# Optimization experiments

Measured on AMD Instinct MI355X. Metric: run time of the kernel, lower is better.

The kernel has to match this reference:

```python
import jax, jax.numpy as jnp
import numpy as np

EPS = 1e-8  # torch F.cosine_similarity default eps
B, T, D = 128, 32, 256
H = 512            # LSTM hidden
S, M = 2048, 64    # memory slots, mem dim
R, W = 4, 1        # read / write heads
OUT = 256


def setup_inputs() -> dict:
    key = jax.random.key(0)
    ks = jax.random.split(key, 12)
    sc = 0.02
    return {
        "x": jax.random.normal(ks[0], (B, T, D), jnp.float32),
        "h0": jnp.zeros((B, H), jnp.float32),
        "c0": jnp.zeros((B, H), jnp.float32),
        "mem0": jax.random.normal(ks[1], (B, S, M), jnp.float32),
        # LSTMCell params (torch gate order i,f,g,o)
        "W_ih": jax.random.normal(ks[2], (4 * H, D), jnp.float32) * sc,
        "W_hh": jax.random.normal(ks[3], (4 * H, H), jnp.float32) * sc,
        "b_ih": jnp.zeros((4 * H,), jnp.float32),
        "b_hh": jnp.zeros((4 * H,), jnp.float32),
        # linear_output: H -> OUT
        "W_out": jax.random.normal(ks[4], (OUT, H), jnp.float32) * 0.001,
        "b_out": jnp.zeros((OUT,), jnp.float32),
        # output_fn: (R*M) -> OUT
        "W_rd": jax.random.normal(ks[5], (OUT, R * M), jnp.float32) * 0.001,
        "b_rd": jnp.zeros((OUT,), jnp.float32),
        # ctrl2head: H -> R*M + R + W*M + W + W*M + W*M
        "W_head": jax.random.normal(ks[6], (R * M + R + 3 * W * M + W, H), jnp.float32) * 0.001,
        "b_head": jnp.zeros((R * M + R + 3 * W * M + W,), jnp.float32),
        "K": 8,
    }


def asp(t, K):
    # top-K sparse masking over last dim (slots); equals torch topk+scatter
    v, idx = jax.lax.top_k(t, K)                       # [B, h, K]
    b = jnp.arange(t.shape[0])[:, None, None]
    h = jnp.arange(t.shape[1])[None, :, None]
    return jnp.zeros_like(t).at[b, h, idx].set(v)


def content_addressing(mem, k, beta):
    # mem [B,S,M], k [B,h,M], beta [B,h,1] -> softmax(beta * cosine_sim) over slots
    dots = jnp.einsum("bhm,bsm->bhs", k, mem)
    kn = jnp.maximum(jnp.linalg.norm(k, axis=-1), EPS)[:, :, None]      # [B,h,1]
    mn = jnp.maximum(jnp.linalg.norm(mem, axis=-1), EPS)[:, None, :]    # [B,1,S]
    cossim = dots / (kn * mn)
    return jax.nn.softmax(beta * cossim, axis=-1)


def dnc_forward(x, h0, c0, mem0, W_ih, W_hh, b_ih, b_hh,
                W_out, b_out, W_rd, b_rd, W_head, b_head, K):
    def step(carry, x_t):
        h, c, mem = carry
        # LSTM cell
        gates = x_t @ W_ih.T + h @ W_hh.T + (b_ih + b_hh)
        i, f, g, o = jnp.split(gates, 4, axis=-1)
        c = jax.nn.sigmoid(f) * c + jax.nn.sigmoid(i) * jnp.tanh(g)
        h = jax.nn.sigmoid(o) * jnp.tanh(c)
        vt = h @ W_out.T + b_out
        # addressing params
        ctrl = h @ W_head.T + b_head
        s = 0
        kr = jnp.tanh(ctrl[:, s:s + R * M]).reshape(-1, R, M); s += R * M
        betar = jax.nn.softplus(ctrl[:, s:s + R]).reshape(-1, R, 1); s += R
        kw = jnp.tanh(ctrl[:, s:s + W * M]).reshape(-1, W, M); s += W * M
        betaw = jax.nn.softplus(ctrl[:, s:s + W]).reshape(-1, W, 1); s += W
        erase = jax.nn.sigmoid(ctrl[:, s:s + W * M]).reshape(-1, W, M); s += W * M
        add = jnp.tanh(ctrl[:, s:s + W * M]).reshape(-1, W, M)
        # write: sparse content addressing, rank-1 erase/add per write head
        ww = asp(content_addressing(mem, kw, betaw), K)     # [B,W,S]
        e = jnp.einsum("bws,bwm->bwsm", ww, erase)
        a = jnp.einsum("bws,bwm->bwsm", ww, add)
        for widx in range(W):
            mem = mem * (1.0 - e[:, widx]) + a[:, widx]
        # read
        wr = asp(content_addressing(mem, kr, betar), K)     # [B,R,S]
        reads = jnp.einsum("brs,bsm->brm", wr, mem)         # [B,R,M]
        out = vt + reads.reshape(reads.shape[0], -1) @ W_rd.T + b_rd
        return (h, c, mem), out

    (_, _, _), outs = jax.lax.scan(step, (h0, c0, mem0), jnp.swapaxes(x, 0, 1))
    return jnp.swapaxes(outs, 0, 1)  # [B, T, OUT]


def reference(x, h0, c0, mem0, W_ih, W_hh, b_ih, b_hh,
              W_out, b_out, W_rd, b_rd, W_head, b_head, K):
    return dnc_forward(x, h0, c0, mem0, W_ih, W_hh, b_ih, b_hh,
                       W_out, b_out, W_rd, b_rd, W_head, b_head, K)
```

## Files before the change

### kernel.cpp

```cpp
#include <hip/hip_runtime.h>
#include <math.h>

#define DEV __device__ __forceinline__

static constexpr int B_ = 128, T_ = 32, H_ = 512;
static constexpr int S_ = 2048, M_ = 64, OUT_ = 256;
static constexpr float EPSF = 1e-8f;

DEV float sigmoidf_(float x){ return 1.0f/(1.0f+expf(-x)); }
DEV float softplusf_(float x){ return fmaxf(x,0.0f) + log1pf(expf(-fabsf(x))); }

DEV unsigned long long packCand(float v, unsigned idx){
  unsigned u = __float_as_uint(v);
  unsigned m = (u & 0x80000000u) ? ~u : (u | 0x80000000u);
  return ((unsigned long long)m << 32) | (unsigned)(~idx);
}
DEV float unpackVal(unsigned long long e){
  unsigned m = (unsigned)(e >> 32);
  unsigned u = (m & 0x80000000u) ? (m & 0x7FFFFFFFu) : ~m;
  return __uint_as_float(u);
}
DEV unsigned unpackIdx(unsigned long long e){ return ~(unsigned)e; }

DEV void cswp(unsigned long long &a, unsigned long long &b){
  if(a < b){ unsigned long long t=a; a=b; b=t; }
}
DEV void sort8(unsigned long long* L){
  cswp(L[0],L[1]); cswp(L[2],L[3]); cswp(L[4],L[5]); cswp(L[6],L[7]);
  cswp(L[0],L[2]); cswp(L[1],L[3]); cswp(L[4],L[6]); cswp(L[5],L[7]);
  cswp(L[1],L[2]); cswp(L[5],L[6]);
  cswp(L[0],L[4]); cswp(L[1],L[5]); cswp(L[2],L[6]); cswp(L[3],L[7]);
  cswp(L[2],L[4]); cswp(L[3],L[5]);
  cswp(L[1],L[2]); cswp(L[3],L[4]); cswp(L[5],L[6]);
}
DEV void bmerge16(unsigned long long* C){
  #pragma unroll
  for(int i=0;i<8;i++) cswp(C[i],C[i+8]);
  #pragma unroll
  for(int g=0;g<2;g++){ int o=g*8;
    cswp(C[o+0],C[o+4]); cswp(C[o+1],C[o+5]); cswp(C[o+2],C[o+6]); cswp(C[o+3],C[o+7]); }
  #pragma unroll
  for(int g=0;g<4;g++){ int o=g*4; cswp(C[o+0],C[o+2]); cswp(C[o+1],C[o+3]); }
  #pragma unroll
  for(int g=0;g<8;g++){ int o=g*2; cswp(C[o],C[o+1]); }
}
DEV void butterfly8(unsigned long long* L, int maxMask){
  for(int mask=1; mask<=maxMask; mask<<=1){
    unsigned long long O[8], C[8];
    #pragma unroll
    for(int i=0;i<8;i++) O[i] = __shfl_xor(L[i], mask, 64);
    #pragma unroll
    for(int i=0;i<8;i++){ unsigned long long a=L[i], b=O[7-i]; C[i] = (a>b)?a:b; }
    cswp(C[0],C[4]); cswp(C[1],C[5]); cswp(C[2],C[6]); cswp(C[3],C[7]);
    cswp(C[0],C[2]); cswp(C[1],C[3]); cswp(C[4],C[6]); cswp(C[5],C[7]);
    cswp(C[0],C[1]); cswp(C[2],C[3]); cswp(C[4],C[5]); cswp(C[6],C[7]);
    #pragma unroll
    for(int i=0;i<8;i++) L[i]=C[i];
  }
}
DEV void butterfly16(unsigned long long* L){
  for(int mask=1; mask<64; mask<<=1){
    unsigned long long O[16], C[16];
    #pragma unroll
    for(int i=0;i<16;i++) O[i] = __shfl_xor(L[i], mask, 64);
    #pragma unroll
    for(int i=0;i<16;i++){ unsigned long long a=L[i], b=O[15-i]; C[i] = (a>b)?a:b; }
    bmerge16(C);
    #pragma unroll
    for(int i=0;i<16;i++) L[i]=C[i];
  }
}

DEV float ctrlv(const float* __restrict__ cp, int b, int jj, const float* __restrict__ bh){
  size_t o = (size_t)b*512 + jj;
  return cp[o] + cp[65536+o] + cp[131072+o] + cp[196608+o] + bh[jj];
}

__global__ __launch_bounds__(256)
void k_gemm64(const float* __restrict__ A, int lda,
              const float* __restrict__ Bm, int ldb,
              float* __restrict__ C, int ldc,
              int kCount,
              const float* __restrict__ bias0, const float* __restrict__ bias1)
{
  const int BM=64, BN=64, BK=16, LDT=68;
  __shared__ float As[BK*LDT];
  __shared__ float Bs[BK*LDT];
  const int m0 = blockIdx.x*BM, n0 = blockIdx.y*BN;
  const int tid = threadIdx.x;
  const int tx = tid & 15, ty = tid >> 4;
  const int kStart = blockIdx.z * kCount;
  float acc[4][4] = {};
  const int row = tid >> 2, kk = (tid & 3) * 4;
  for(int k0 = kStart; k0 < kStart + kCount; k0 += BK){
    float4 av = *(const float4*)(A  + (size_t)(m0+row)*lda + k0 + kk);
    float4 bv = *(const float4*)(Bm + (size_t)(n0+row)*ldb + k0 + kk);
    As[(kk+0)*LDT+row]=av.x; As[(kk+1)*LDT+row]=av.y; As[(kk+2)*LDT+row]=av.z; As[(kk+3)*LDT+row]=av.w;
    Bs[(kk+0)*LDT+row]=bv.x; Bs[(kk+1)*LDT+row]=bv.y; Bs[(kk+2)*LDT+row]=bv.z; Bs[(kk+3)*LDT+row]=bv.w;
    __syncthreads();
    #pragma unroll
    for(int k=0;k<BK;k++){
      float4 a = *(const float4*)&As[k*LDT + 4*ty];
      float4 b = *(const float4*)&Bs[k*LDT + 4*tx];
      acc[0][0]+=a.x*b.x; acc[0][1]+=a.x*b.y; acc[0][2]+=a.x*b.z; acc[0][3]+=a.x*b.w;
      acc[1][0]+=a.y*b.x; acc[1][1]+=a.y*b.y; acc[1][2]+=a.y*b.z; acc[1][3]+=a.y*b.w;
      acc[2][0]+=a.z*b.x; acc[2][1]+=a.z*b.y; acc[2][2]+=a.z*b.z; acc[2][3]+=a.z*b.w;
      acc[3][0]+=a.w*b.x; acc[3][1]+=a.w*b.y; acc[3][2]+=a.w*b.z; acc[3][3]+=a.w*b.w;
    }
    __syncthreads();
  }
  float* Cz = C + (size_t)blockIdx.z * (size_t)gridDim.x * BM * (size_t)ldc;
  #pragma unroll
  for(int i=0;i<4;i++){
    int m = m0 + 4*ty + i;
    int n = n0 + 4*tx;
    float4 o; o.x=acc[i][0]; o.y=acc[i][1]; o.z=acc[i][2]; o.w=acc[i][3];
    if(bias0){
      o.x += bias0[n]+bias1[n];     o.y += bias0[n+1]+bias1[n+1];
      o.z += bias0[n+2]+bias1[n+2]; o.w += bias0[n+3]+bias1[n+3];
    }
    *(float4*)(Cz + (size_t)m*ldc + n) = o;
  }
}

__global__ __launch_bounds__(256)
void k_L1(const float* __restrict__ hprev, const float* __restrict__ Whh,
          float* __restrict__ gparts, int tG,
          const float* __restrict__ hv,
          const float* __restrict__ Wout, const float* __restrict__ Whead,
          float* __restrict__ ctrlW, float* __restrict__ vtpW, int tV,
          float* __restrict__ memC, const float* __restrict__ ctrlH,
          const float* __restrict__ bhead,
          const unsigned long long* __restrict__ candW,
          const unsigned long long* __restrict__ candR,
          const float* __restrict__ statsB,
          float* __restrict__ readsAll, int tH)
{
  __shared__ __align__(16) float smem[2304];
  const int blk = blockIdx.x, tid = threadIdx.x;

  if(blk < 256){
    if(tG < 0) return;
    float* As = smem;
    float* Bs = smem + 1088;
    const int z = blk >> 6, rem = blk & 63;
    const int m0 = (rem & 1)*64, n0 = (rem >> 1)*64;
    const int tx = tid & 15, ty = tid >> 4;
    float acc[4][4] = {};
    const int row = tid >> 2, kq = (tid & 3)*4;
    const int kStart = z*128;
    for(int k0 = kStart; k0 < kStart + 128; k0 += 16){
      float4 av = *(const float4*)(hprev + (size_t)(m0+row)*512 + k0 + kq);
      float4 bv = *(const float4*)(Whh   + (size_t)(n0+row)*512 + k0 + kq);
      As[(kq+0)*68+row]=av.x; As[(kq+1)*68+row]=av.y; As[(kq+2)*68+row]=av.z; As[(kq+3)*68+row]=av.w;
      Bs[(kq+0)*68+row]=bv.x; Bs[(kq+1)*68+row]=bv.y; Bs[(kq+2)*68+row]=bv.z; Bs[(kq+3)*68+row]=bv.w;
      __syncthreads();
      #pragma unroll
      for(int k=0;k<16;k++){
        float4 a = *(const float4*)&As[k*68 + 4*ty];
        float4 b = *(const float4*)&Bs[k*68 + 4*tx];
        acc[0][0]+=a.x*b.x; acc[0][1]+=a.x*b.y; acc[0][2]+=a.x*b.z; acc[0][3]+=a.x*b.w;
        acc[1][0]+=a.y*b.x; acc[1][1]+=a.y*b.y; acc[1][2]+=a.y*b.z; acc[1][3]+=a.y*b.w;
        acc[2][0]+=a.z*b.x; acc[2][1]+=a.z*b.y; acc[2][2]+=a.z*b.z; acc[2][3]+=a.z*b.w;
        acc[3][0]+=a.w*b.x; acc[3][1]+=a.w*b.y; acc[3][2]+=a.w*b.z; acc[3][3]+=a.w*b.w;
      }
      __syncthreads();
    }
    float* Cz = gparts + (size_t)z*262144;
    #pragma unroll
    for(int i=0;i<4;i++){
      float4 o; o.x=acc[i][0]; o.y=acc[i][1]; o.z=acc[i][2]; o.w=acc[i][3];
      *(float4*)(Cz + (size_t)(m0+4*ty+i)*2048 + n0 + 4*tx) = o;
    }
    return;
  }

  if(blk < 320){
    if(tV < 0) return;
    float* As = smem;
    float* Bs = smem + 1088;
    const int g = blk - 256;
    const int z = g >> 4, rem = g & 15;
    const int m0 = (rem & 1)*64;
    const int jj0 = (rem >> 1)*64;
    const int tx = tid & 15, ty = tid >> 4;
    float acc[4][4] = {};
    const int row = tid >> 2, kq = (tid & 3)*4;
    const int kStart = z*128;
    const int jr = jj0 + row;
    const float* Bsrc = (jr < 453) ? (Whead + (size_t)jr*512) : nullptr;
    for(int k0 = kStart; k0 < kStart + 128; k0 += 16){
      float4 av = *(const float4*)(hv + (size_t)(m0+row)*512 + k0 + kq);
      float4 bv = make_float4(0.f,0.f,0.f,0.f);
      if(Bsrc) bv = *(const float4*)(Bsrc + k0 + kq);
      As[(kq+0)*68+row]=av.x; As[(kq+1)*68+row]=av.y; As[(kq+2)*68+row]=av.z; As[(kq+3)*68+row]=av.w;
      Bs[(kq+0)*68+row]=bv.x; Bs[(kq+1)*68+row]=bv.y; Bs[(kq+2)*68+row]=bv.z; Bs[(kq+3)*68+row]=bv.w;
      __syncthreads();
      #pragma unroll
      for(int k=0;k<16;k++){
        float4 a = *(const float4*)&As[k*68 + 4*ty];
        float4 b = *(const float4*)&Bs[k*68 + 4*tx];
        acc[0][0]+=a.x*b.x; acc[0][1]+=a.x*b.y; acc[0][2]+=a.x*b.z; acc[0][3]+=a.x*b.w;
        acc[1][0]+=a.y*b.x; acc[1][1]+=a.y*b.y; acc[1][2]+=a.y*b.z; acc[1][3]+=a.y*b.w;
        acc[2][0]+=a.z*b.x; acc[2][1]+=a.z*b.y; acc[2][2]+=a.z*b.z; acc[2][3]+=a.z*b.w;
        acc[3][0]+=a.w*b.x; acc[3][1]+=a.w*b.y; acc[3][2]+=a.w*b.z; acc[3][3]+=a.w*b.w;
      }
      __syncthreads();
    }
    float* Cz = ctrlW + (size_t)z*65536;
    #pragma unroll
    for(int i=0;i<4;i++){
      float4 o; o.x=acc[i][0]; o.y=acc[i][1]; o.z=acc[i][2]; o.w=acc[i][3];
      *(float4*)(Cz + (size_t)(m0+4*ty+i)*512 + jj0 + 4*tx) = o;
    }
    return;
  }

  if(blk < 448){
    if(tH < 0) return;
    float* kr     = smem;
    float* nv     = smem + 256;
    float* oldrow = smem + 768;
    float* er     = smem + 1280;
    float* ad     = smem + 1344;
    float* coefR  = smem + 1408;
    int*   widx   = (int*)(smem + 1412);
    float* wval   = smem + 1420;

    const int b = blk - 320;
    const int lane = tid & 63, wave = tid >> 6;
    const size_t memb = (size_t)b*(size_t)S_*M_;

    kr[tid] = tanhf(ctrlv(ctrlH, b, tid, bhead));
    if(tid < 64){
      er[tid] = sigmoidf_(ctrlv(ctrlH, b, 325+tid, bhead));
      ad[tid] = tanhf(ctrlv(ctrlH, b, 389+tid, bhead));
    }
    __syncthreads();

    if(wave == 0){
      float smx[4], ssm[4];
      #pragma unroll
      for(int c2=0;c2<4;c2++){
        const float* st = statsB + (((size_t)b*4 + c2)*5 + 4)*2;
        smx[c2] = st[0]; ssm[c2] = st[1];
      }
      float mxw = fmaxf(fmaxf(smx[0],smx[1]), fmaxf(smx[2],smx[3]));
      float Zw = ssm[0]*expf(smx[0]-mxw) + ssm[1]*expf(smx[1]-mxw)
               + ssm[2]*expf(smx[2]-mxw) + ssm[3]*expf(smx[3]-mxw);
      unsigned long long L[8];
      L[0] = (lane < 32) ? candW[((size_t)b*4 + (lane>>3))*8 + (lane&7)] : 0ULL;
      #pragma unroll
      for(int j=1;j<8;j++) L[j] = 0ULL;
      butterfly8(L, 16);
      if(lane == 0){
        float invZ = 1.0f / Zw;
        #pragma unroll
        for(int p=0;p<8;p++){
          widx[p] = (int)unpackIdx(L[p]);
          wval[p] = expf(unpackVal(L[p]) - mxw) * invZ;
        }
      }
    } else if(wave == 1 && lane < 4){
      float s = 0.f;
      #pragma unroll
      for(int m=0;m<64;m++){ float x = kr[lane*64+m]; s += x*x; }
      coefR[lane] = softplusf_(ctrlv(ctrlH, b, 256+lane, bhead)) / fmaxf(sqrtf(s), EPSF);
    }
    __syncthreads();

    {
      int j = tid >> 6, m = tid & 63;
      #pragma unroll
      for(int p=0;p<2;p++){
        int idx = tid + p*256;
        int jj = idx >> 6, mm = idx & 63;
        int s = widx[jj];
        float w = wval[jj];
        size_t ptr = memb + (size_t)s*M_ + mm;
        float old = memC[ptr];
        oldrow[jj*64+mm] = old;
        float x = old * (1.0f - w*er[mm]) + w*ad[mm];
        memC[ptr] = x;
        nv[jj*64+mm] = x;
      }
      (void)j; (void)m;
    }
    __syncthreads();

    {
      const int r = wave;
      const int sW = lane & 7, g = lane >> 3;
      const float4* nv4 = (const float4*)nv;
      const float4* ov4 = (const float4*)oldrow;
      const float4* kr4 = (const float4*)kr;
      float4 na = nv4[sW*16 + g*2], nb2 = nv4[sW*16 + g*2 + 1];
      float4 oa = ov4[sW*16 + g*2], ob = ov4[sW*16 + g*2 + 1];
      float4 ka = kr4[r*16  + g*2], kb = kr4[r*16  + g*2 + 1];
      float dot = na.x*ka.x + na.y*ka.y + na.z*ka.z + na.w*ka.w
                + nb2.x*kb.x + nb2.y*kb.y + nb2.z*kb.z + nb2.w*kb.w;
      float n2  = na.x*na.x + na.y*na.y + na.z*na.z + na.w*na.w
                + nb2.x*nb2.x + nb2.y*nb2.y + nb2.z*nb2.z + nb2.w*nb2.w;
      float odot= oa.x*ka.x + oa.y*ka.y + oa.z*ka.z + oa.w*ka.w
                + ob.x*kb.x + ob.y*kb.y + ob.z*kb.z + ob.w*kb.w;
      float on2 = oa.x*oa.x + oa.y*oa.y + oa.z*oa.z + oa.w*oa.w
                + ob.x*ob.x + ob.y*ob.y + ob.z*ob.z + ob.w*ob.w;
      #pragma unroll
      for(int mask=8; mask<64; mask<<=1){
        dot  += __shfl_xor(dot,  mask, 64);
        n2   += __shfl_xor(n2,   mask, 64);
        odot += __shfl_xor(odot, mask, 64);
        on2  += __shfl_xor(on2,  mask, 64);
      }
      float fixv = coefR[r] * dot  / fmaxf(sqrtf(n2),  EPSF);
      float oldv = coefR[r] * odot / fmaxf(sqrtf(on2), EPSF);
      int myw = widx[sW];

      float scx[4], scs[4];
      #pragma unroll
      for(int c2=0;c2<4;c2++){
        const float* st = statsB + (((size_t)b*4 + c2)*5 + r)*2;
        scx[c2] = st[0]; scs[c2] = st[1];
      }
      float mxp = fmaxf(fmaxf(scx[0],scx[1]), fmaxf(scx[2],scx[3]));

      unsigned long long L[8];
      {
        int c2 = lane >> 4, rank = lane & 15;
        unsigned long long eA = candR[(((size_t)b*4 + c2)*4 + r)*16 + rank];
        unsigned idxA = unpackIdx(eA);
        bool kill = false;
        #pragma unroll
        for(int p=0;p<8;p++) kill = kill || (idxA == (unsigned)widx[p]);
        if(kill) eA = 0ULL;
        unsigned long long eB = (lane < 8) ? packCand(fixv, (unsigned)myw) : 0ULL;
        L[0] = (eA > eB) ? eA : eB;
        L[1] = (eA > eB) ? eB : eA;
        #pragma unroll
        for(int j2=2;j2<8;j2++) L[j2] = 0ULL;
      }
      butterfly8(L, 32);

      float mxS = fmaxf(mxp, unpackVal(L[0]));
      float Zp = scs[0]*expf(scx[0]-mxS) + scs[1]*expf(scx[1]-mxS)
               + scs[2]*expf(scx[2]-mxS) + scs[3]*expf(scx[3]-mxS);
      float adj = (lane < 8) ? (expf(fixv - mxS) - expf(oldv - mxS)) : 0.f;
      #pragma unroll
      for(int mask=1; mask<64; mask<<=1) adj += __shfl_xor(adj, mask, 64);
      float invZ = 1.0f / (Zp + adj);

      float acc = 0.f;
      #pragma unroll
      for(int p=0;p<8;p++){
        float w = expf(unpackVal(L[p]) - mxS) * invZ;
        int si = (int)unpackIdx(L[p]);
        acc += w * memC[memb + (size_t)si*M_ + lane];
      }
      readsAll[((size_t)b*T_ + tH)*256 + r*64 + lane] = acc;
    }
    return;
  }

  if(tV < 0) return;
  {
    float* As = smem;
    float* Bs = smem + 1088;
    const int g = blk - 448;
    const int z = g >> 3, rem = g & 7;
    const int m0 = (rem & 1)*64, n0 = (rem >> 1)*64;
    const int tx = tid & 15, ty = tid >> 4;
    float acc[4][4] = {};
    const int row = tid >> 2, kq = (tid & 3)*4;
    const int kStart = z*128;
    const float* Bsrc = Wout + (size_t)(n0+row)*512;
    for(int k0 = kStart; k0 < kStart + 128; k0 += 16){
      float4 av = *(const float4*)(hv + (size_t)(m0+row)*512 + k0 + kq);
      float4 bv = *(const float4*)(Bsrc + k0 + kq);
      As[(kq+0)*68+row]=av.x; As[(kq+1)*68+row]=av.y; As[(kq+2)*68+row]=av.z; As[(kq+3)*68+row]=av.w;
      Bs[(kq+0)*68+row]=bv.x; Bs[(kq+1)*68+row]=bv.y; Bs[(kq+2)*68+row]=bv.z; Bs[(kq+3)*68+row]=bv.w;
      __syncthreads();
      #pragma unroll
      for(int k=0;k<16;k++){
        float4 a = *(const float4*)&As[k*68 + 4*ty];
        float4 b = *(const float4*)&Bs[k*68 + 4*tx];
        acc[0][0]+=a.x*b.x; acc[0][1]+=a.x*b.y; acc[0][2]+=a.x*b.z; acc[0][3]+=a.x*b.w;
        acc[1][0]+=a.y*b.x; acc[1][1]+=a.y*b.y; acc[1][2]+=a.y*b.z; acc[1][3]+=a.y*b.w;
        acc[2][0]+=a.z*b.x; acc[2][1]+=a.z*b.y; acc[2][2]+=a.z*b.z; acc[2][3]+=a.z*b.w;
        acc[3][0]+=a.w*b.x; acc[3][1]+=a.w*b.y; acc[3][2]+=a.w*b.z; acc[3][3]+=a.w*b.w;
      }
      __syncthreads();
    }
    float* Cz = vtpW + (size_t)z*32768;
    #pragma unroll
    for(int i=0;i<4;i++){
      float4 o; o.x=acc[i][0]; o.y=acc[i][1]; o.z=acc[i][2]; o.w=acc[i][3];
      *(float4*)(Cz + (size_t)(m0+4*ty+i)*256 + n0 + 4*tx) = o;
    }
  }
}

__global__ __launch_bounds__(512)
void k_L2(const float* __restrict__ xg, const float* __restrict__ gp,
          float* __restrict__ hout, float* __restrict__ c, int tL,
          const float* __restrict__ memC, const float* __restrict__ ctrlS,
          const float* __restrict__ bhead,
          unsigned long long* __restrict__ candW,
          unsigned long long* __restrict__ candR,
          float* __restrict__ statsB, int tS,
          const float* __restrict__ vtpR, const float* __restrict__ bout,
          float* __restrict__ out)
{
  __shared__ float smem[2896];
  const int blk = blockIdx.x, tid = threadIdx.x;

  if(blk >= 640){
    if(tS < 0) return;
    int idx = (blk - 640)*512 + tid;
    int b = idx >> 8, n = idx & 255;
    float s = vtpR[(size_t)b*256+n] + vtpR[32768 + (size_t)b*256+n]
            + vtpR[65536 + (size_t)b*256+n] + vtpR[98304 + (size_t)b*256+n];
    out[((size_t)b*T_ + tS)*OUT_ + n] = s + bout[n];
    return;
  }
  if(blk >= 512){
    if(tL < 0) return;
    int idx = (blk - 512)*512 + tid;
    int b = idx >> 9, j = idx & 511;
    const float* xr = xg + ((size_t)b*T_ + tL)*(size_t)(4*H_);
    float gi = xr[j], gf = xr[512+j], gg = xr[1024+j], go = xr[1536+j];
    #pragma unroll
    for(int s4=0;s4<4;s4++){
      const float* pr = gp + ((size_t)s4*B_ + b)*(size_t)(4*H_);
      gi += pr[j]; gf += pr[512+j]; gg += pr[1024+j]; go += pr[1536+j];
    }
    float cc = sigmoidf_(gf)*c[idx] + sigmoidf_(gi)*tanhf(gg);
    float hh = sigmoidf_(go)*tanhf(cc);
    c[idx] = cc; hout[idx] = hh;
    return;
  }

  if(tS < 0) return;
  float* kk   = smem;
  float* coef = smem + 320;
  float* tile = smem + 328;
  const int b = blk >> 2, ch = blk & 3;
  const int lane = tid & 63, wid = tid >> 6;
  if(tid < 256) kk[tid] = tanhf(ctrlv(ctrlS, b, tid, bhead));
  else if(tid < 320) kk[tid] = tanhf(ctrlv(ctrlS, b, tid+4, bhead));
  __syncthreads();
  if(tid < 5){
    float s = 0.f;
    #pragma unroll
    for(int m=0;m<64;m++){ float x = kk[tid*64+m]; s += x*x; }
    float beta = softplusf_( tid<4 ? ctrlv(ctrlS, b, 256+tid, bhead)
                                   : ctrlv(ctrlS, b, 324, bhead) );
    coef[tid] = beta / fmaxf(sqrtf(s), EPSF);
  }
  __syncthreads();

  {
    const int s = ch*512 + tid;
    const float4* row = (const float4*)(memC + ((size_t)b*S_ + s)*M_);
    float nrm=0.f, d0=0.f, d1=0.f, d2=0.f, d3=0.f, dw=0.f;
    #pragma unroll
    for(int r4=0;r4<16;r4++){
      float4 xa = row[r4];
      float av[4] = {xa.x,xa.y,xa.z,xa.w};
      #pragma unroll
      for(int j=0;j<4;j++){
        const int m = r4*4+j;
        float a = av[j];
        nrm += a*a;
        d0 += a*kk[m];     d1 += a*kk[64+m]; d2 += a*kk[128+m];
        d3 += a*kk[192+m]; dw += a*kk[256+m];
      }
    }
    float inv = 1.0f / fmaxf(sqrtf(nrm), EPSF);
    tile[0*512+tid] = coef[0]*d0*inv;
    tile[1*512+tid] = coef[1]*d1*inv;
    tile[2*512+tid] = coef[2]*d2*inv;
    tile[3*512+tid] = coef[3]*d3*inv;
    tile[4*512+tid] = coef[4]*dw*inv;
  }
  __syncthreads();

  if(wid < 4){
    unsigned long long L[16];
    #pragma unroll
    for(int j=0;j<8;j++){
      int i = lane + j*64;
      L[j] = packCand(tile[wid*512 + i], (unsigned)(ch*512 + i));
    }
    sort8(L);
    #pragma unroll
    for(int j=8;j<16;j++) L[j] = 0ULL;
    butterfly16(L);
    if(lane == 0){
      unsigned long long* dst = candR + (((size_t)b*4 + ch)*4 + wid)*16;
      #pragma unroll
      for(int j=0;j<16;j++) dst[j] = L[j];
    }
  } else if(wid == 4){
    unsigned long long L[8];
    #pragma unroll
    for(int j=0;j<8;j++){
      int i = lane + j*64;
      L[j] = packCand(tile[4*512 + i], (unsigned)(ch*512 + i));
    }
    sort8(L);
    butterfly8(L, 32);
    if(lane == 0){
      unsigned long long* dst = candW + ((size_t)b*4 + ch)*8;
      #pragma unroll
      for(int j=0;j<8;j++) dst[j] = L[j];
    }
  } else {
    int h0 = (wid==5) ? 0 : (wid==6) ? 2 : 4;
    int nh = (wid==7) ? 1 : 2;
    for(int q=0;q<nh;q++){
      int h = h0 + q;
      float x[8];
      #pragma unroll
      for(int j=0;j<8;j++) x[j] = tile[h*512 + lane + j*64];
      float mx = x[0];
      #pragma unroll
      for(int j=1;j<8;j++) mx = fmaxf(mx, x[j]);
      #pragma unroll
      for(int mask=1; mask<64; mask<<=1) mx = fmaxf(mx, __shfl_xor(mx, mask, 64));
      float sm = 0.f;
      #pragma unroll
      for(int j=0;j<8;j++) sm += expf(x[j]-mx);
      #pragma unroll
      for(int mask=1; mask<64; mask<<=1) sm += __shfl_xor(sm, mask, 64);
      if(lane == 0){
        float* st = statsB + (((size_t)b*4 + ch)*5 + h)*2;
        st[0] = mx; st[1] = sm;
      }
    }
  }
}

__global__ __launch_bounds__(256)
void k_outg(const float* __restrict__ A,
            const float* __restrict__ Wrd,
            const float* __restrict__ brd,
            float* __restrict__ out)
{
  const int BK=16, LDT=68;
  __shared__ float As[BK*LDT];
  __shared__ float Bs[BK*LDT];
  const int m0 = blockIdx.x*64, n0 = blockIdx.y*64;
  const int tid = threadIdx.x;
  const int tx = tid & 15, ty = tid >> 4;
  float acc[4][4] = {};
  const int row = tid >> 2, kk = (tid & 3) * 4;
  for(int k0 = 0; k0 < 256; k0 += BK){
    float4 av = *(const float4*)(A   + (size_t)(m0+row)*256 + k0 + kk);
    float4 bv = *(const float4*)(Wrd + (size_t)(n0+row)*256 + k0 + kk);
    As[(kk+0)*LDT+row]=av.x; As[(kk+1)*LDT+row]=av.y; As[(kk+2)*LDT+row]=av.z; As[(kk+3)*LDT+row]=av.w;
    Bs[(kk+0)*LDT+row]=bv.x; Bs[(kk+1)*LDT+row]=bv.y; Bs[(kk+2)*LDT+row]=bv.z; Bs[(kk+3)*LDT+row]=bv.w;
    __syncthreads();
    #pragma unroll
    for(int k=0;k<BK;k++){
      float4 a = *(const float4*)&As[k*LDT + 4*ty];
      float4 b = *(const float4*)&Bs[k*LDT + 4*tx];
      acc[0][0]+=a.x*b.x; acc[0][1]+=a.x*b.y; acc[0][2]+=a.x*b.z; acc[0][3]+=a.x*b.w;
      acc[1][0]+=a.y*b.x; acc[1][1]+=a.y*b.y; acc[1][2]+=a.y*b.z; acc[1][3]+=a.y*b.w;
      acc[2][0]+=a.z*b.x; acc[2][1]+=a.z*b.y; acc[2][2]+=a.z*b.z; acc[2][3]+=a.z*b.w;
      acc[3][0]+=a.w*b.x; acc[3][1]+=a.w*b.y; acc[3][2]+=a.w*b.z; acc[3][3]+=a.w*b.w;
    }
    __syncthreads();
  }
  const int nb = n0 + 4*tx;
  float4 bb = *(const float4*)(brd + nb);
  #pragma unroll
  for(int i=0;i<4;i++){
    int m = m0 + 4*ty + i;
    float4 vt = *(const float4*)(out + (size_t)m*256 + nb);
    float4 o;
    o.x = acc[i][0] + bb.x + vt.x;
    o.y = acc[i][1] + bb.y + vt.y;
    o.z = acc[i][2] + bb.z + vt.z;
    o.w = acc[i][3] + bb.w + vt.w;
    *(float4*)(out + (size_t)m*256 + nb) = o;
  }
}

extern "C" void kernel_launch(void* const* d_in, const int* in_sizes, int n_in,
                              void* d_out, int out_size, void* d_ws, size_t ws_size,
                              hipStream_t stream)
{
  const float* x     = (const float*)d_in[0];
  const float* h0    = (const float*)d_in[1];
  const float* c0    = (const float*)d_in[2];
  const float* mem0  = (const float*)d_in[3];
  const float* W_ih  = (const float*)d_in[4];
  const float* W_hh  = (const float*)d_in[5];
  const float* b_ih  = (const float*)d_in[6];
  const float* b_hh  = (const float*)d_in[7];
  const float* W_out = (const float*)d_in[8];
  const float* b_out = (const float*)d_in[9];
  const float* W_rd  = (const float*)d_in[10];
  const float* b_rd  = (const float*)d_in[11];
  const float* W_head= (const float*)d_in[12];
  const float* b_head= (const float*)d_in[13];
  float* out = (float*)d_out;

  float* ws     = (float*)d_ws;
  float* memC   = ws;
  float* xg     = memC  + 16777216;
  float* hbuf   = xg    + 8388608;
  float* c      = hbuf  + 131072;
  float* gparts = c     + 65536;
  float* ctrlP  = gparts+ 1048576;
  float* vtp    = ctrlP + 524288;
  float* reads_all = vtp + 262144;
  unsigned long long* candW = (unsigned long long*)(reads_all + 1048576);
  unsigned long long* candR = candW + 4096;
  float* statsB = (float*)(candR + 32768);
  const size_t need = (size_t)(28324864) * sizeof(float);
  if(ws_size < need) return;

  hipMemcpyAsync(c, c0, 65536*sizeof(float), hipMemcpyDeviceToDevice, stream);
  hipMemcpyAsync(memC, mem0, (size_t)16777216*sizeof(float), hipMemcpyDeviceToDevice, stream);
  k_gemm64<<<dim3(64,32,1),256,0,stream>>>(x,256, W_ih,256, xg,2048, 256, b_ih,b_hh);

  for(int tau=0; tau<=33; ++tau){
    int tG = (tau < 32) ? tau : -1;
    int tV = (tau >= 1 && tau <= 32) ? tau-1 : -1;
    int tH = (tau >= 2) ? tau-2 : -1;
    const float* hprev = (tau == 0) ? h0 : hbuf + (size_t)((tau-1)&1)*65536;
    const float* hv    = (tV >= 0) ? hbuf + (size_t)(tV&1)*65536 : hbuf;
    float* ctrlW       = ctrlP + (size_t)((tV >= 0 ? tV : 0)&1)*262144;
    float* vtpW        = vtp   + (size_t)((tV >= 0 ? tV : 0)&1)*131072;
    const float* ctrlH = ctrlP + (size_t)((tH >= 0 ? tH : 0)&1)*262144;
    k_L1<<<480,256,0,stream>>>(hprev, W_hh, gparts, tG,
                               hv, W_out, W_head, ctrlW, vtpW, tV,
                               memC, ctrlH, b_head, candW, candR, statsB,
                               reads_all, tH);
    if(tau <= 32){
      int tL = (tau < 32) ? tau : -1;
      int tS = (tau >= 1) ? tau-1 : -1;
      float* hout        = hbuf  + (size_t)((tL >= 0 ? tL : 0)&1)*65536;
      const float* ctrlS = ctrlP + (size_t)((tS >= 0 ? tS : 0)&1)*262144;
      const float* vtpR  = vtp   + (size_t)((tS >= 0 ? tS : 0)&1)*131072;
      k_L2<<<704,512,0,stream>>>(xg, gparts, hout, c, tL,
                                 memC, ctrlS, b_head, candW, candR, statsB, tS,
                                 vtpR, b_out, out);
    }
  }
  k_outg<<<dim3(64,4),256,0,stream>>>(reads_all, W_rd, b_rd, out);
}
```

Measured before the change: 1.402 ms.

## Fuse per-step input projection GEMM into the L1 step kernel

Removes the standalone up-front x·W_ih GEMM over all timesteps and computes each timestep's input projection inside k_L1 with 128 extra blocks, split-K into two partial buffers that k_L2 sums. This eliminates one large kernel launch and the big xg buffer, and shrinks the workspace. In exchange each step's k_L1 grid grows, which may lengthen the per-step critical path, and k_L2 now reads two partials.

```diff
diff --git a/kernel.cpp b/kernel.cpp
--- a/kernel.cpp
+++ b/kernel.cpp
@@ -74,53 +74,6 @@
 DEV float ctrlv(const float* __restrict__ cp, int b, int jj, const float* __restrict__ bh){
   size_t o = (size_t)b*512 + jj;
   return cp[o] + cp[65536+o] + cp[131072+o] + cp[196608+o] + bh[jj];
-}
-
-__global__ __launch_bounds__(256)
-void k_gemm64(const float* __restrict__ A, int lda,
-              const float* __restrict__ Bm, int ldb,
-              float* __restrict__ C, int ldc,
-              int kCount,
-              const float* __restrict__ bias0, const float* __restrict__ bias1)
-{
-  const int BM=64, BN=64, BK=16, LDT=68;
-  __shared__ float As[BK*LDT];
-  __shared__ float Bs[BK*LDT];
-  const int m0 = blockIdx.x*BM, n0 = blockIdx.y*BN;
-  const int tid = threadIdx.x;
-  const int tx = tid & 15, ty = tid >> 4;
-  const int kStart = blockIdx.z * kCount;
-  float acc[4][4] = {};
-  const int row = tid >> 2, kk = (tid & 3) * 4;
-  for(int k0 = kStart; k0 < kStart + kCount; k0 += BK){
-    float4 av = *(const float4*)(A  + (size_t)(m0+row)*lda + k0 + kk);
-    float4 bv = *(const float4*)(Bm + (size_t)(n0+row)*ldb + k0 + kk);
-    As[(kk+0)*LDT+row]=av.x; As[(kk+1)*LDT+row]=av.y; As[(kk+2)*LDT+row]=av.z; As[(kk+3)*LDT+row]=av.w;
-    Bs[(kk+0)*LDT+row]=bv.x; Bs[(kk+1)*LDT+row]=bv.y; Bs[(kk+2)*LDT+row]=bv.z; Bs[(kk+3)*LDT+row]=bv.w;
-    __syncthreads();
-    #pragma unroll
-    for(int k=0;k<BK;k++){
-      float4 a = *(const float4*)&As[k*LDT + 4*ty];
-      float4 b = *(const float4*)&Bs[k*LDT + 4*tx];
-      acc[0][0]+=a.x*b.x; acc[0][1]+=a.x*b.y; acc[0][2]+=a.x*b.z; acc[0][3]+=a.x*b.w;
-      acc[1][0]+=a.y*b.x; acc[1][1]+=a.y*b.y; acc[1][2]+=a.y*b.z; acc[1][3]+=a.y*b.w;
-      acc[2][0]+=a.z*b.x; acc[2][1]+=a.z*b.y; acc[2][2]+=a.z*b.z; acc[2][3]+=a.z*b.w;
-      acc[3][0]+=a.w*b.x; acc[3][1]+=a.w*b.y; acc[3][2]+=a.w*b.z; acc[3][3]+=a.w*b.w;
-    }
-    __syncthreads();
-  }
-  float* Cz = C + (size_t)blockIdx.z * (size_t)gridDim.x * BM * (size_t)ldc;
-  #pragma unroll
-  for(int i=0;i<4;i++){
-    int m = m0 + 4*ty + i;
-    int n = n0 + 4*tx;
-    float4 o; o.x=acc[i][0]; o.y=acc[i][1]; o.z=acc[i][2]; o.w=acc[i][3];
-    if(bias0){
-      o.x += bias0[n]+bias1[n];     o.y += bias0[n+1]+bias1[n+1];
-      o.z += bias0[n+2]+bias1[n+2]; o.w += bias0[n+3]+bias1[n+3];
-    }
-    *(float4*)(Cz + (size_t)m*ldc + n) = o;
-  }
 }
 
 __global__ __launch_bounds__(256)
@@ -134,7 +87,10 @@
           const unsigned long long* __restrict__ candW,
           const unsigned long long* __restrict__ candR,
           const float* __restrict__ statsB,
-          float* __restrict__ readsAll, int tH)
+          float* __restrict__ readsAll, int tH,
+          const float* __restrict__ x, const float* __restrict__ Wih,
+          const float* __restrict__ bih, const float* __restrict__ bhh,
+          float* __restrict__ xgp)
 {
   __shared__ __align__(16) float smem[2304];
   const int blk = blockIdx.x, tid = threadIdx.x;
@@ -264,13 +220,12 @@
     } else if(wave == 1 && lane < 4){
       float s = 0.f;
       #pragma unroll
-      for(int m=0;m<64;m++){ float x = kr[lane*64+m]; s += x*x; }
+      for(int m=0;m<64;m++){ float x2 = kr[lane*64+m]; s += x2*x2; }
       coefR[lane] = softplusf_(ctrlv(ctrlH, b, 256+lane, bhead)) / fmaxf(sqrtf(s), EPSF);
     }
     __syncthreads();
 
     {
-      int j = tid >> 6, m = tid & 63;
       #pragma unroll
       for(int p=0;p<2;p++){
         int idx = tid + p*256;
@@ -280,11 +235,10 @@
         size_t ptr = memb + (size_t)s*M_ + mm;
         float old = memC[ptr];
         oldrow[jj*64+mm] = old;
-        float x = old * (1.0f - w*er[mm]) + w*ad[mm];
-        memC[ptr] = x;
-        nv[jj*64+mm] = x;
-      }
-      (void)j; (void)m;
+        float x2 = old * (1.0f - w*er[mm]) + w*ad[mm];
+        memC[ptr] = x2;
+        nv[jj*64+mm] = x2;
+      }
     }
     __syncthreads();
 
@@ -361,8 +315,8 @@
     return;
   }
 
-  if(tV < 0) return;
-  {
+  if(blk < 480){
+    if(tV < 0) return;
     float* As = smem;
     float* Bs = smem + 1088;
     const int g = blk - 448;
@@ -396,11 +350,56 @@
       float4 o; o.x=acc[i][0]; o.y=acc[i][1]; o.z=acc[i][2]; o.w=acc[i][3];
       *(float4*)(Cz + (size_t)(m0+4*ty+i)*256 + n0 + 4*tx) = o;
     }
+    return;
+  }
+
+  if(tG < 0) return;
+  {
+    float* As = smem;
+    float* Bs = smem + 1088;
+    const int g = blk - 480;
+    const int z = g >> 6, rem = g & 63;
+    const int mb = (rem & 1)*64;
+    const int n0 = (rem >> 1)*64;
+    const int tx = tid & 15, ty = tid >> 4;
+    float acc[4][4] = {};
+    const int row = tid >> 2, kq = (tid & 3)*4;
+    const int kStart = z*128;
+    for(int k0 = kStart; k0 < kStart + 128; k0 += 16){
+      float4 av = *(const float4*)(x   + ((size_t)(mb+row)*T_ + tG)*256 + k0 + kq);
+      float4 bv = *(const float4*)(Wih + (size_t)(n0+row)*256 + k0 + kq);
+      As[(kq+0)*68+row]=av.x; As[(kq+1)*68+row]=av.y; As[(kq+2)*68+row]=av.z; As[(kq+3)*68+row]=av.w;
+      Bs[(kq+0)*68+row]=bv.x; Bs[(kq+1)*68+row]=bv.y; Bs[(kq+2)*68+row]=bv.z; Bs[(kq+3)*68+row]=bv.w;
+      __syncthreads();
+      #pragma unroll
+      for(int k=0;k<16;k++){
+        float4 a = *(const float4*)&As[k*68 + 4*ty];
+        float4 b = *(const float4*)&Bs[k*68 + 4*tx];
+        acc[0][0]+=a.x*b.x; acc[0][1]+=a.x*b.y; acc[0][2]+=a.x*b.z; acc[0][3]+=a.x*b.w;
+        acc[1][0]+=a.y*b.x; acc[1][1]+=a.y*b.y; acc[1][2]+=a.y*b.z; acc[1][3]+=a.y*b.w;
+        acc[2][0]+=a.z*b.x; acc[2][1]+=a.z*b.y; acc[2][2]+=a.z*b.z; acc[2][3]+=a.z*b.w;
+        acc[3][0]+=a.w*b.x; acc[3][1]+=a.w*b.y; acc[3][2]+=a.w*b.z; acc[3][3]+=a.w*b.w;
+      }
+      __syncthreads();
+    }
+    const int nb = n0 + 4*tx;
+    float bias[4] = {0.f,0.f,0.f,0.f};
+    if(z == 0){
+      #pragma unroll
+      for(int j2=0;j2<4;j2++){ int n = nb + j2; bias[j2] = bih[n] + bhh[n]; }
+    }
+    float* Cz = xgp + (size_t)z*262144;
+    #pragma unroll
+    for(int i=0;i<4;i++){
+      float4 o; o.x=acc[i][0]+bias[0]; o.y=acc[i][1]+bias[1];
+      o.z=acc[i][2]+bias[2]; o.w=acc[i][3]+bias[3];
+      *(float4*)(Cz + (size_t)(mb+4*ty+i)*2048 + nb) = o;
+    }
   }
 }
 
 __global__ __launch_bounds__(512)
-void k_L2(const float* __restrict__ xg, const float* __restrict__ gp,
+void k_L2(const float* __restrict__ xgp, const float* __restrict__ gp,
           float* __restrict__ hout, float* __restrict__ c, int tL,
           const float* __restrict__ memC, const float* __restrict__ ctrlS,
           const float* __restrict__ bhead,
@@ -426,8 +425,12 @@
     if(tL < 0) return;
     int idx = (blk - 512)*512 + tid;
     int b = idx >> 9, j = idx & 511;
-    const float* xr = xg + ((size_t)b*T_ + tL)*(size_t)(4*H_);
-    float gi = xr[j], gf = xr[512+j], gg = xr[1024+j], go = xr[1536+j];
+    const float* x0 = xgp + (size_t)b*2048;
+    const float* x1 = xgp + 262144 + (size_t)b*2048;
+    float gi = x0[j]      + x1[j];
+    float gf = x0[512+j]  + x1[512+j];
+    float gg = x0[1024+j] + x1[1024+j];
+    float go = x0[1536+j] + x1[1536+j];
     #pragma unroll
     for(int s4=0;s4<4;s4++){
       const float* pr = gp + ((size_t)s4*B_ + b)*(size_t)(4*H_);
@@ -451,7 +454,7 @@
   if(tid < 5){
     float s = 0.f;
     #pragma unroll
-    for(int m=0;m<64;m++){ float x = kk[tid*64+m]; s += x*x; }
+    for(int m=0;m<64;m++){ float x2 = kk[tid*64+m]; s += x2*x2; }
     float beta = softplusf_( tid<4 ? ctrlv(ctrlS, b, 256+tid, bhead)
                                    : ctrlv(ctrlS, b, 324, bhead) );
     coef[tid] = beta / fmaxf(sqrtf(s), EPSF);
@@ -519,17 +522,17 @@
     int nh = (wid==7) ? 1 : 2;
     for(int q=0;q<nh;q++){
       int h = h0 + q;
-      float x[8];
-      #pragma unroll
-      for(int j=0;j<8;j++) x[j] = tile[h*512 + lane + j*64];
-      float mx = x[0];
-      #pragma unroll
-      for(int j=1;j<8;j++) mx = fmaxf(mx, x[j]);
+      float x2[8];
+      #pragma unroll
+      for(int j=0;j<8;j++) x2[j] = tile[h*512 + lane + j*64];
+      float mx = x2[0];
+      #pragma unroll
+      for(int j=1;j<8;j++) mx = fmaxf(mx, x2[j]);
       #pragma unroll
       for(int mask=1; mask<64; mask<<=1) mx = fmaxf(mx, __shfl_xor(mx, mask, 64));
       float sm = 0.f;
       #pragma unroll
-      for(int j=0;j<8;j++) sm += expf(x[j]-mx);
+      for(int j=0;j<8;j++) sm += expf(x2[j]-mx);
       #pragma unroll
       for(int mask=1; mask<64; mask<<=1) sm += __shfl_xor(sm, mask, 64);
       if(lane == 0){
@@ -608,8 +611,8 @@
 
   float* ws     = (float*)d_ws;
   float* memC   = ws;
-  float* xg     = memC  + 16777216;
-  float* hbuf   = xg    + 8388608;
+  float* xgp    = memC  + 16777216;
+  float* hbuf   = xgp   + 524288;
   float* c      = hbuf  + 131072;
   float* gparts = c     + 65536;
   float* ctrlP  = gparts+ 1048576;
@@ -618,12 +621,11 @@
   unsigned long long* candW = (unsigned long long*)(reads_all + 1048576);
   unsigned long long* candR = candW + 4096;
   float* statsB = (float*)(candR + 32768);
-  const size_t need = (size_t)(28324864) * sizeof(float);
+  const size_t need = (size_t)(20460544) * sizeof(float);
   if(ws_size < need) return;
 
   hipMemcpyAsync(c, c0, 65536*sizeof(float), hipMemcpyDeviceToDevice, stream);
   hipMemcpyAsync(memC, mem0, (size_t)16777216*sizeof(float), hipMemcpyDeviceToDevice, stream);
-  k_gemm64<<<dim3(64,32,1),256,0,stream>>>(x,256, W_ih,256, xg,2048, 256, b_ih,b_hh);
 
   for(int tau=0; tau<=33; ++tau){
     int tG = (tau < 32) ? tau : -1;
@@ -634,17 +636,18 @@
     float* ctrlW       = ctrlP + (size_t)((tV >= 0 ? tV : 0)&1)*262144;
     float* vtpW        = vtp   + (size_t)((tV >= 0 ? tV : 0)&1)*131072;
     const float* ctrlH = ctrlP + (size_t)((tH >= 0 ? tH : 0)&1)*262144;
-    k_L1<<<480,256,0,stream>>>(hprev, W_hh, gparts, tG,
+    k_L1<<<608,256,0,stream>>>(hprev, W_hh, gparts, tG,
                                hv, W_out, W_head, ctrlW, vtpW, tV,
                                memC, ctrlH, b_head, candW, candR, statsB,
-                               reads_all, tH);
+                               reads_all, tH,
+                               x, W_ih, b_ih, b_hh, xgp);
     if(tau <= 32){
       int tL = (tau < 32) ? tau : -1;
       int tS = (tau >= 1) ? tau-1 : -1;
       float* hout        = hbuf  + (size_t)((tL >= 0 ? tL : 0)&1)*65536;
       const float* ctrlS = ctrlP + (size_t)((tS >= 0 ? tS : 0)&1)*262144;
       const float* vtpR  = vtp   + (size_t)((tS >= 0 ? tS : 0)&1)*131072;
-      k_L2<<<704,512,0,stream>>>(xg, gparts, hout, c, tL,
+      k_L2<<<704,512,0,stream>>>(xgp, gparts, hout, c, tL,
                                  memC, ctrlS, b_head, candW, candR, statsB, tS,
                                  vtpR, b_out, out);
     }
```

Result: slower. 1.454 ms (+3.7%).
